# Performance work log

Measured on AMD Instinct MI355X. Metric: run time of the kernel, lower is better.

## Reference

```python
import jax, jax.numpy as jnp
import numpy as np

N = 50000
E = 800000
IN_C = 128
HID = 64
HEADS = 4
NUM_CLASSES = 10
NUM_GRAPHS = 64
EPS = 1e-5
NEG_SLOPE = 0.2


def setup_inputs() -> dict:
    key = jax.random.key(0)
    ks = jax.random.split(key, 32)
    inp = {}
    inp["x"] = jax.random.normal(ks[0], (N, IN_C), dtype=jnp.float32)
    inp["edge_index"] = jax.random.randint(ks[1], (2, E), 0, N, dtype=jnp.int32)
    inp["batch"] = jnp.sort(jax.random.randint(ks[2], (N,), 0, NUM_GRAPHS, dtype=jnp.int32))
    s = 0.05
    # GATConv1: in=128 -> heads=4, hid=64, concat -> 256
    inp["W1"] = jax.random.normal(ks[3], (IN_C, HEADS * HID), dtype=jnp.float32) * s
    inp["a_src1"] = jax.random.normal(ks[4], (HEADS, HID), dtype=jnp.float32) * s
    inp["a_dst1"] = jax.random.normal(ks[5], (HEADS, HID), dtype=jnp.float32) * s
    inp["b1"] = jnp.zeros((HEADS * HID,), dtype=jnp.float32)
    inp["g1"] = jnp.ones((HEADS * HID,), dtype=jnp.float32)
    inp["be1"] = jnp.zeros((HEADS * HID,), dtype=jnp.float32)
    # GATConv2: in=256 -> heads=4, hid=64, concat -> 256
    inp["W2"] = jax.random.normal(ks[6], (HEADS * HID, HEADS * HID), dtype=jnp.float32) * s
    inp["a_src2"] = jax.random.normal(ks[7], (HEADS, HID), dtype=jnp.float32) * s
    inp["a_dst2"] = jax.random.normal(ks[8], (HEADS, HID), dtype=jnp.float32) * s
    inp["b2"] = jnp.zeros((HEADS * HID,), dtype=jnp.float32)
    inp["g2"] = jnp.ones((HEADS * HID,), dtype=jnp.float32)
    inp["be2"] = jnp.zeros((HEADS * HID,), dtype=jnp.float32)
    # GATConv3: in=256 -> heads=1, hid=64, mean (concat=False) -> 64
    inp["W3"] = jax.random.normal(ks[9], (HEADS * HID, 1 * HID), dtype=jnp.float32) * s
    inp["a_src3"] = jax.random.normal(ks[10], (1, HID), dtype=jnp.float32) * s
    inp["a_dst3"] = jax.random.normal(ks[11], (1, HID), dtype=jnp.float32) * s
    inp["b3"] = jnp.zeros((HID,), dtype=jnp.float32)
    inp["g3"] = jnp.ones((HID,), dtype=jnp.float32)
    inp["be3"] = jnp.zeros((HID,), dtype=jnp.float32)
    # final classifier
    inp["fcW"] = jax.random.normal(ks[12], (HID, NUM_CLASSES), dtype=jnp.float32) * s
    inp["fcb"] = jnp.zeros((NUM_CLASSES,), dtype=jnp.float32)
    return inp


def gat_conv(x, src, dst, W, a_src, a_dst, b, heads, out_c, concat):
    # Linear transform, split heads: [N, H, C]
    h = (x @ W).reshape(-1, heads, out_c)
    # Per-node attention logits (dot with per-head attention vectors): [N, H]
    as_ = jnp.einsum("nhc,hc->nh", h, a_src)
    ad_ = jnp.einsum("nhc,hc->nh", h, a_dst)
    # Per-edge unnormalized attention (src contributes a_src, dst a_dst)
    e = jax.nn.leaky_relu(as_[src] + ad_[dst], NEG_SLOPE)  # [E, H]
    # Segment softmax over destination node (stable)
    e_max = jax.ops.segment_max(e, dst, num_segments=N)  # [N, H]
    ex = jnp.exp(e - e_max[dst])
    denom = jax.ops.segment_sum(ex, dst, num_segments=N)  # [N, H]
    alpha = ex / denom[dst]  # [E, H]
    # Weighted scatter-aggregate of source features
    msg = h[src] * alpha[:, :, None]  # [E, H, C]
    out = jax.ops.segment_sum(msg, dst, num_segments=N)  # [N, H, C]
    out = out.reshape(-1, heads * out_c) if concat else out.mean(axis=1)
    return out + b


def batch_norm(x, gamma, beta):
    mean = x.mean(axis=0)
    var = x.var(axis=0)
    return (x - mean) * jax.lax.rsqrt(var + EPS) * gamma + beta


def reference(x, edge_index, batch, W1, a_src1, a_dst1, b1, g1, be1,
              W2, a_src2, a_dst2, b2, g2, be2,
              W3, a_src3, a_dst3, b3, g3, be3, fcW, fcb):
    src, dst = edge_index[0], edge_index[1]
    h = jax.nn.relu(gat_conv(x, src, dst, W1, a_src1, a_dst1, b1, HEADS, HID, True))
    h = batch_norm(h, g1, be1)  # dropout = identity (eval)
    h = jax.nn.relu(gat_conv(h, src, dst, W2, a_src2, a_dst2, b2, HEADS, HID, True))
    h = batch_norm(h, g2, be2)
    h = jax.nn.relu(gat_conv(h, src, dst, W3, a_src3, a_dst3, b3, 1, HID, False))
    h = batch_norm(h, g3, be3)
    # global mean pool over graphs
    sums = jax.ops.segment_sum(h, batch, num_segments=NUM_GRAPHS)  # [G, HID]
    counts = jax.ops.segment_sum(jnp.ones((h.shape[0],), h.dtype), batch, num_segments=NUM_GRAPHS)
    pooled = sums / jnp.maximum(counts, 1.0)[:, None]
    return pooled @ fcW + fcb
```

## Files before the change

### kernel.cpp

```cpp
#include <hip/hip_runtime.h>
#include <hip/hip_bf16.h>

#define N_NODES 50000
#define NUM_E   800000
#define EPS_BN  1e-5f
#define NUM_GRAPHS 64

typedef __attribute__((ext_vector_type(8))) short bf16x8;
typedef __attribute__((ext_vector_type(4))) float f32x4;
typedef unsigned short ushort_t;
typedef unsigned int uint_t;

static __device__ __forceinline__ unsigned short f2bf(float f) {
    unsigned int u = __float_as_uint(f);
    u += 0x7fffu + ((u >> 16) & 1u);
    return (unsigned short)(u >> 16);
}
static __device__ __forceinline__ uint_t pkbf(float lo, float hi) {
    __hip_bfloat162 t = __float22bfloat162_rn(make_float2(lo, hi));
    return *(uint_t*)&t;
}
static __device__ __forceinline__ float bflo(uint_t u) { return __uint_as_float(u << 16); }
static __device__ __forceinline__ float bfhi(uint_t u) { return __uint_as_float(u & 0xffff0000u); }

__global__ void hist_kernel(const int* __restrict__ ei, int* __restrict__ deg) {
    int e = blockIdx.x * blockDim.x + threadIdx.x;
    if (e >= NUM_E) return;
    atomicAdd(&deg[ei[NUM_E + e]], 1);
}

__global__ void scan_local_kernel(const int* __restrict__ deg, int* __restrict__ rowptr,
                                  int* __restrict__ bsum) {
    __shared__ int ws[4];
    int b = blockIdx.x, t = threadIdx.x;
    int i = b * 256 + t;
    int lane = t & 63, wv = t >> 6;
    int v = (i < N_NODES) ? deg[i] : 0;
    int incl = v;
#pragma unroll
    for (int off = 1; off < 64; off <<= 1) {
        int u = __shfl_up(incl, off, 64);
        if (lane >= off) incl += u;
    }
    if (lane == 63) ws[wv] = incl;
    __syncthreads();
    if (t == 0) {
        int s = 0;
#pragma unroll
        for (int k = 0; k < 4; ++k) { int x = ws[k]; ws[k] = s; s += x; }
        bsum[b] = s;
    }
    __syncthreads();
    if (i < N_NODES) rowptr[i + 1] = ws[wv] + incl;
}

__global__ void scan_sums_kernel(int* __restrict__ bsum, int nb) {
    __shared__ int ws[4];
    int t = threadIdx.x;
    int lane = t & 63, wv = t >> 6;
    int v = (t < nb) ? bsum[t] : 0;
    int incl = v;
#pragma unroll
    for (int off = 1; off < 64; off <<= 1) {
        int u = __shfl_up(incl, off, 64);
        if (lane >= off) incl += u;
    }
    if (lane == 63) ws[wv] = incl;
    __syncthreads();
    if (t == 0) {
        int s = 0;
#pragma unroll
        for (int k = 0; k < 4; ++k) { int x = ws[k]; ws[k] = s; s += x; }
    }
    __syncthreads();
    if (t < nb) bsum[t] = ws[wv] + incl - v;
}

__global__ void scan_add_kernel(int* __restrict__ rowptr, const int* __restrict__ bsum) {
    int b = blockIdx.x, t = threadIdx.x;
    int i = b * 256 + t;
    if (i < N_NODES) rowptr[i + 1] += bsum[b];
    if (b == 0 && t == 0) rowptr[0] = 0;
}

__global__ void scatter_kernel(const int* __restrict__ ei, const int* __restrict__ rowptr,
                               int* __restrict__ fill, int* __restrict__ srcs) {
    int e = blockIdx.x * blockDim.x + threadIdx.x;
    if (e >= NUM_E) return;
    int dst = ei[NUM_E + e];
    int pos = rowptr[dst] + atomicAdd(&fill[dst], 1);
    srcs[pos] = ei[e];
}

__global__ void batch_offsets_kernel(const int* __restrict__ batch, int* __restrict__ goff) {
    int g = threadIdx.x;
    if (g > NUM_GRAPHS) return;
    int lo = 0, hi = N_NODES;
    while (lo < hi) {
        int mid = (lo + hi) >> 1;
        if (batch[mid] < g) lo = mid + 1; else hi = mid;
    }
    goff[g] = lo;
}

__global__ void prep_all_kernel(const float* __restrict__ W1, const float* __restrict__ W2,
                                const float* __restrict__ W3, const float* __restrict__ x,
                                ushort_t* __restrict__ w1t, ushort_t* __restrict__ w2t,
                                ushort_t* __restrict__ w3t, ushort_t* __restrict__ xbf) {
    const int S1 = 128 * 256, S2 = 256 * 256, S3 = 256 * 64;
    const int SW = S1 + S2 + S3;
    const int SX = N_NODES * 128 / 4;
    int i = blockIdx.x * blockDim.x + threadIdx.x;
    if (i < SX) {
        float4 v = ((const float4*)x)[i];
        ((uint2*)xbf)[i] = make_uint2(pkbf(v.x, v.y), pkbf(v.z, v.w));
    } else if (i < SX + SW) {
        int j = i - SX;
        if (j < S1) {
            int k = j / 256, n = j % 256;
            w1t[n * 128 + k] = f2bf(W1[j]);
        } else if (j < S1 + S2) {
            int jj = j - S1; int k = jj / 256, n = jj % 256;
            w2t[n * 256 + k] = f2bf(W2[jj]);
        } else {
            int jj = j - S1 - S2; int k = jj / 64, n = jj % 64;
            w3t[n * 256 + k] = f2bf(W3[jj]);
        }
    }
}

__global__ __launch_bounds__(256) void scale_w_kernel(const float* __restrict__ stats,
                                                      const float* __restrict__ g,
                                                      const float* __restrict__ be,
                                                      const ushort_t* __restrict__ wt,
                                                      ushort_t* __restrict__ wts,
                                                      float* __restrict__ cvec) {
    int n = blockIdx.x, k = threadIdx.x;
    float m = stats[k] * (1.f / N_NODES);
    float var = fmaxf(stats[256 + k] * (1.f / N_NODES) - m * m, 0.f);
    float rs = rsqrtf(var + EPS_BN) * g[k];
    float b = be[k] - m * rs;
    float wv = bflo((uint_t)wt[n * 256 + k]);
    wts[n * 256 + k] = f2bf(rs * wv);
    float p = b * wv;
    __shared__ float ws[4];
    int lane = k & 63, wid = k >> 6;
#pragma unroll
    for (int off = 1; off < 64; off <<= 1) p += __shfl_xor(p, off, 64);
    if (lane == 0) ws[wid] = p;
    __syncthreads();
    if (k == 0) cvec[n] = ws[0] + ws[1] + ws[2] + ws[3];
}

template<int K, int NFULL, int BN>
__global__ __launch_bounds__(256) void gemm_fused_kernel(const ushort_t* __restrict__ A,
                                                         const ushort_t* __restrict__ Bt,
                                                         ushort_t* __restrict__ C,
                                                         const float* __restrict__ cvec,
                                                         const float* __restrict__ a_src,
                                                         const float* __restrict__ a_dst,
                                                         float* __restrict__ as_,
                                                         float* __restrict__ ad_) {
    const int NT = BN / 16;
    const int NG = BN / 64;
    constexpr int LOOP_BYTES = (128 * 40 + BN * 40) * 2;
    constexpr int EPI_BYTES  = 4 * 32 * 64 * 2;
    constexpr int SMEM_BYTES = LOOP_BYTES > EPI_BYTES ? LOOP_BYTES : EPI_BYTES;
    __shared__ __align__(16) unsigned char smem[SMEM_BYTES];
    ushort_t (*As)[40]     = (ushort_t (*)[40])smem;
    ushort_t (*Bs)[40]     = (ushort_t (*)[40])(smem + 128 * 40 * 2);
    ushort_t (*Cs)[32][64] = (ushort_t (*)[32][64])smem;
    __shared__ float cvec_s[BN];
    __shared__ float asrc_s[BN], adst_s[BN];
    int tid = threadIdx.x;
    int lane = tid & 63, w = tid >> 6;
    int row0 = blockIdx.x * 128, col0 = blockIdx.y * BN;
    int m_l = lane & 15, q = lane >> 4;

    if (tid < BN) {
        cvec_s[tid] = cvec[col0 + tid];
        asrc_s[tid] = a_src[col0 + tid];
        adst_s[tid] = a_dst[col0 + tid];
    }
    __syncthreads();

    f32x4 acc[2][NT];
#pragma unroll
    for (int r = 0; r < 2; ++r)
#pragma unroll
        for (int c = 0; c < NT; ++c) acc[r][c] = (f32x4){0.f, 0.f, 0.f, 0.f};

    int ar = tid >> 1, ako = (tid & 1) * 16;

    for (int k0 = 0; k0 < K; k0 += 32) {
        int gr = row0 + ar;
        uint4 u0 = make_uint4(0, 0, 0, 0), u1 = make_uint4(0, 0, 0, 0);
        if (gr < N_NODES) {
            const ushort_t* ap = A + (long)gr * K + k0 + ako;
            u0 = *(const uint4*)ap;
            u1 = *(const uint4*)(ap + 8);
        }
        if constexpr (BN == 128) {
            int br = tid >> 1, bko = (tid & 1) * 16;
            const ushort_t* bp = Bt + (long)(col0 + br) * K + k0 + bko;
            uint4 b0 = *(const uint4*)bp;
            uint4 b1 = *(const uint4*)(bp + 8);
            *(uint4*)&As[ar][ako] = u0;
            *(uint4*)&As[ar][ako + 8] = u1;
            *(uint4*)&Bs[br][bko] = b0;
            *(uint4*)&Bs[br][bko + 8] = b1;
        } else {
            int br = tid >> 2, bko = (tid & 3) * 8;
            uint4 bv = *(const uint4*)(Bt + (long)(col0 + br) * K + k0 + bko);
            *(uint4*)&As[ar][ako] = u0;
            *(uint4*)&As[ar][ako + 8] = u1;
            *(uint4*)&Bs[br][bko] = bv;
        }
        __syncthreads();

        bf16x8 af[2];
#pragma unroll
        for (int r = 0; r < 2; ++r)
            af[r] = *(const bf16x8*)&As[w * 32 + r * 16 + m_l][q * 8];
#pragma unroll
        for (int c = 0; c < NT; ++c) {
            bf16x8 bf = *(const bf16x8*)&Bs[c * 16 + m_l][q * 8];
#pragma unroll
            for (int r = 0; r < 2; ++r)
                acc[r][c] = __builtin_amdgcn_mfma_f32_16x16x32_bf16(af[r], bf, acc[r][c], 0, 0, 0);
        }
        __syncthreads();
    }

    const int H = NFULL / 64;
#pragma unroll
    for (int gblk = 0; gblk < NG; ++gblk) {
        int hidx = blockIdx.y * NG + gblk;
        int colg = col0 + gblk * 64;
#pragma unroll
        for (int r = 0; r < 2; ++r)
#pragma unroll
            for (int cc = 0; cc < 4; ++cc)
#pragma unroll
                for (int i = 0; i < 4; ++i)
                    Cs[w][r * 16 + q * 4 + i][cc * 16 + m_l] =
                        f2bf(acc[r][gblk * 4 + cc][i] + cvec_s[gblk * 64 + cc * 16 + m_l]);
#pragma unroll
        for (int j = 0; j < 4; ++j) {
            int flat = j * 64 + lane;
            int lr = flat >> 3, chg = flat & 7;
            int gr = row0 + w * 32 + lr;
            uint4 u = *(uint4*)&Cs[w][lr][chg * 8];
            float f0 = bflo(u.x), f1 = bfhi(u.x), f2 = bflo(u.y), f3 = bfhi(u.y);
            float f4 = bflo(u.z), f5 = bfhi(u.z), f6 = bflo(u.w), f7 = bfhi(u.w);
            int cb = gblk * 64 + chg * 8;
            float s1 = f0 * asrc_s[cb] + f1 * asrc_s[cb + 1] + f2 * asrc_s[cb + 2] + f3 * asrc_s[cb + 3]
                     + f4 * asrc_s[cb + 4] + f5 * asrc_s[cb + 5] + f6 * asrc_s[cb + 6] + f7 * asrc_s[cb + 7];
            float s2 = f0 * adst_s[cb] + f1 * adst_s[cb + 1] + f2 * adst_s[cb + 2] + f3 * adst_s[cb + 3]
                     + f4 * adst_s[cb + 4] + f5 * adst_s[cb + 5] + f6 * adst_s[cb + 6] + f7 * adst_s[cb + 7];
#pragma unroll
            for (int o = 1; o < 8; o <<= 1) {
                s1 += __shfl_xor(s1, o, 64);
                s2 += __shfl_xor(s2, o, 64);
            }
            if (gr < N_NODES) {
                *(uint4*)(C + (long)gr * NFULL + colg + chg * 8) = u;
                if ((lane & 7) == 0) {
                    as_[gr * H + hidx] = s1;
                    ad_[gr * H + hidx] = s2;
                }
            }
        }
    }
}

__global__ __launch_bounds__(256) void agg4_kernel(const ushort_t* __restrict__ h,
                                                   const float* __restrict__ as_,
                                                   const float* __restrict__ ad_,
                                                   const int* __restrict__ rowptr,
                                                   const int* __restrict__ srcs,
                                                   const float* __restrict__ bias,
                                                   ushort_t* __restrict__ out) {
    __shared__ float4 alf[4][4][17];
    __shared__ int    sed[4][4][17];
    int tid = threadIdx.x;
    int lane = tid & 63, w = tid >> 6;
    int q = lane >> 4, cl = lane & 15;
    int n = blockIdx.x * 16 + w * 4 + q;

    int start = rowptr[n];
    int deg = rowptr[n + 1] - start;

    float4 adv = *(const float4*)(ad_ + n * 4);
    float ad4[4] = {adv.x, adv.y, adv.z, adv.w};

    float mx[4] = {-1e30f, -1e30f, -1e30f, -1e30f};
    float dn[4] = {0.f, 0.f, 0.f, 0.f};
    {
        float vst[4] = {-1e30f, -1e30f, -1e30f, -1e30f};
        int s0 = 0;
        if (deg > 0) s0 = srcs[start + min(cl, deg - 1)];
        sed[w][q][cl] = s0;
        if (cl < deg) {
            float4 av = *(const float4*)(as_ + s0 * 4);
            float vv[4] = {av.x + ad4[0], av.y + ad4[1], av.z + ad4[2], av.w + ad4[3]};
#pragma unroll
            for (int hh = 0; hh < 4; ++hh) {
                float v = vv[hh] > 0.f ? vv[hh] : 0.2f * vv[hh];
                vst[hh] = v; mx[hh] = v; dn[hh] = 1.f;
            }
        }
        alf[w][q][cl] = make_float4(vst[0], vst[1], vst[2], vst[3]);
        for (int j = cl + 16; j < deg; j += 16) {
            int s = srcs[start + j];
            float4 av = *(const float4*)(as_ + s * 4);
            float vv[4] = {av.x + ad4[0], av.y + ad4[1], av.z + ad4[2], av.w + ad4[3]};
#pragma unroll
            for (int hh = 0; hh < 4; ++hh) {
                float v = vv[hh] > 0.f ? vv[hh] : 0.2f * vv[hh];
                float mn = fmaxf(mx[hh], v);
                dn[hh] = dn[hh] * __expf(mx[hh] - mn) + __expf(v - mn);
                mx[hh] = mn;
            }
        }
    }
    float mloc[4] = {mx[0], mx[1], mx[2], mx[3]};
#pragma unroll
    for (int off = 1; off < 16; off <<= 1)
#pragma unroll
        for (int hh = 0; hh < 4; ++hh) mx[hh] = fmaxf(mx[hh], __shfl_xor(mx[hh], off, 64));
#pragma unroll
    for (int hh = 0; hh < 4; ++hh) dn[hh] *= __expf(mloc[hh] - mx[hh]);
#pragma unroll
    for (int off = 1; off < 16; off <<= 1)
#pragma unroll
        for (int hh = 0; hh < 4; ++hh) dn[hh] += __shfl_xor(dn[hh], off, 64);
    float inv[4];
#pragma unroll
    for (int hh = 0; hh < 4; ++hh) inv[hh] = dn[hh] > 0.f ? 1.f / dn[hh] : 0.f;
    {
        float4 vv = alf[w][q][cl];
        alf[w][q][cl] = make_float4(__expf(vv.x - mx[0]) * inv[0], __expf(vv.y - mx[1]) * inv[1],
                                    __expf(vv.z - mx[2]) * inv[2], __expf(vv.w - mx[3]) * inv[3]);
    }

    int hd = cl >> 2, cbase = cl * 16;
    float acc[16];
#pragma unroll
    for (int k = 0; k < 16; ++k) acc[k] = 0.f;

    for (int chunk = 0; chunk < deg || chunk == 0; chunk += 16) {
        if (chunk > 0) {
            int j = chunk + cl;
            int s = srcs[start + min(j, deg - 1)];
            sed[w][q][cl] = s;
            float a4[4] = {0.f, 0.f, 0.f, 0.f};
            if (j < deg) {
                float4 av = *(const float4*)(as_ + s * 4);
                float vv[4] = {av.x + ad4[0], av.y + ad4[1], av.z + ad4[2], av.w + ad4[3]};
#pragma unroll
                for (int hh = 0; hh < 4; ++hh) {
                    float v = vv[hh] > 0.f ? vv[hh] : 0.2f * vv[hh];
                    a4[hh] = __expf(v - mx[hh]) * inv[hh];
                }
            }
            alf[w][q][cl] = make_float4(a4[0], a4[1], a4[2], a4[3]);
        }
        int cnt = min(16, deg - chunk);
        if (cnt < 0) cnt = 0;
        int e = 0;
        for (; e + 4 <= cnt; e += 4) {
            float av[4]; int sv[4];
#pragma unroll
            for (int t = 0; t < 4; ++t) {
                av[t] = ((const float*)&alf[w][q][e + t])[hd];
                sv[t] = sed[w][q][e + t];
            }
            uint4 ua[4];
#pragma unroll
            for (int t = 0; t < 4; ++t)
                ua[t] = *(const uint4*)(h + (long)sv[t] * 256 + cbase);
#pragma unroll
            for (int t = 0; t < 4; ++t) {
                float al = av[t];
                acc[0] += al * bflo(ua[t].x); acc[1] += al * bfhi(ua[t].x);
                acc[2] += al * bflo(ua[t].y); acc[3] += al * bfhi(ua[t].y);
                acc[4] += al * bflo(ua[t].z); acc[5] += al * bfhi(ua[t].z);
                acc[6] += al * bflo(ua[t].w); acc[7] += al * bfhi(ua[t].w);
            }
#pragma unroll
            for (int t = 0; t < 4; ++t)
                ua[t] = *(const uint4*)(h + (long)sv[t] * 256 + cbase + 8);
#pragma unroll
            for (int t = 0; t < 4; ++t) {
                float al = av[t];
                acc[8]  += al * bflo(ua[t].x); acc[9]  += al * bfhi(ua[t].x);
                acc[10] += al * bflo(ua[t].y); acc[11] += al * bfhi(ua[t].y);
                acc[12] += al * bflo(ua[t].z); acc[13] += al * bfhi(ua[t].z);
                acc[14] += al * bflo(ua[t].w); acc[15] += al * bfhi(ua[t].w);
            }
        }
        for (; e < cnt; ++e) {
            float al = ((const float*)&alf[w][q][e])[hd];
            const ushort_t* hr = h + (long)sed[w][q][e] * 256 + cbase;
            uint4 u0 = *(const uint4*)hr;
            uint4 u1 = *(const uint4*)(hr + 8);
            acc[0]  += al * bflo(u0.x); acc[1]  += al * bfhi(u0.x);
            acc[2]  += al * bflo(u0.y); acc[3]  += al * bfhi(u0.y);
            acc[4]  += al * bflo(u0.z); acc[5]  += al * bfhi(u0.z);
            acc[6]  += al * bflo(u0.w); acc[7]  += al * bfhi(u0.w);
            acc[8]  += al * bflo(u1.x); acc[9]  += al * bfhi(u1.x);
            acc[10] += al * bflo(u1.y); acc[11] += al * bfhi(u1.y);
            acc[12] += al * bflo(u1.z); acc[13] += al * bfhi(u1.z);
            acc[14] += al * bflo(u1.w); acc[15] += al * bfhi(u1.w);
        }
        if (deg <= 16) break;
    }

    uint_t ow[8];
#pragma unroll
    for (int t = 0; t < 8; ++t) {
        float lo = fmaxf(acc[t * 2] + bias[cbase + t * 2], 0.f);
        float hi = fmaxf(acc[t * 2 + 1] + bias[cbase + t * 2 + 1], 0.f);
        ow[t] = pkbf(lo, hi);
    }
    ushort_t* op = out + (long)n * 256 + cbase;
    *(uint4*)op = make_uint4(ow[0], ow[1], ow[2], ow[3]);
    *(uint4*)(op + 8) = make_uint4(ow[4], ow[5], ow[6], ow[7]);
}

__global__ __launch_bounds__(256) void agg1_kernel(const ushort_t* __restrict__ h,
                                                   const float* __restrict__ as_,
                                                   const float* __restrict__ ad_,
                                                   const int* __restrict__ rowptr,
                                                   const int* __restrict__ srcs,
                                                   const float* __restrict__ bias,
                                                   ushort_t* __restrict__ out,
                                                   float* __restrict__ stats) {
    __shared__ float alf1[4][8][9];
    __shared__ int   sed1[4][8][9];
    __shared__ float ssum[64], ssq[64];
    int tid = threadIdx.x;
    int lane = tid & 63, w = tid >> 6;
    int o = lane >> 3, cl = lane & 7;
    int n = blockIdx.x * 32 + w * 8 + o;
    bool valid = n < N_NODES;
    int nc = valid ? n : N_NODES - 1;
    if (tid < 64) { ssum[tid] = 0.f; ssq[tid] = 0.f; }
    __syncthreads();

    int start = rowptr[nc];
    int deg = valid ? rowptr[nc + 1] - start : 0;
    float adn = ad_[nc];

    float mx = -1e30f, dn = 0.f;
    {
        float vst = -1e30f;
        int s0 = 0;
        if (deg > 0) s0 = srcs[start + min(cl, deg - 1)];
        sed1[w][o][cl] = s0;
        if (cl < deg) {
            float v = as_[s0] + adn;
            v = v > 0.f ? v : 0.2f * v;
            vst = v; mx = v; dn = 1.f;
        }
        alf1[w][o][cl] = vst;
        for (int j = cl + 8; j < deg; j += 8) {
            int s = srcs[start + j];
            float v = as_[s] + adn;
            v = v > 0.f ? v : 0.2f * v;
            float mn = fmaxf(mx, v);
            dn = dn * __expf(mx - mn) + __expf(v - mn);
            mx = mn;
        }
    }
    float mloc = mx;
#pragma unroll
    for (int off = 1; off < 8; off <<= 1) mx = fmaxf(mx, __shfl_xor(mx, off, 64));
    dn *= __expf(mloc - mx);
#pragma unroll
    for (int off = 1; off < 8; off <<= 1) dn += __shfl_xor(dn, off, 64);
    float inv = dn > 0.f ? 1.f / dn : 0.f;

    alf1[w][o][cl] = __expf(alf1[w][o][cl] - mx) * inv;

    int c0 = cl * 8;
    float acc[8] = {0.f, 0.f, 0.f, 0.f, 0.f, 0.f, 0.f, 0.f};

    for (int chunk = 0; chunk < deg || chunk == 0; chunk += 8) {
        if (chunk > 0) {
            int j = chunk + cl;
            int s = srcs[start + min(j, deg - 1)];
            sed1[w][o][cl] = s;
            float al = 0.f;
            if (j < deg) {
                float v = as_[s] + adn;
                v = v > 0.f ? v : 0.2f * v;
                al = __expf(v - mx) * inv;
            }
            alf1[w][o][cl] = al;
        }
        int cnt = min(8, deg - chunk);
        if (cnt < 0) cnt = 0;
        int e = 0;
        for (; e + 4 <= cnt; e += 4) {
            float av[4]; int sv[4];
#pragma unroll
            for (int t = 0; t < 4; ++t) {
                av[t] = alf1[w][o][e + t];
                sv[t] = sed1[w][o][e + t];
            }
            uint4 ua[4];
#pragma unroll
            for (int t = 0; t < 4; ++t)
                ua[t] = *(const uint4*)(h + (long)sv[t] * 64 + c0);
#pragma unroll
            for (int t = 0; t < 4; ++t) {
                float al = av[t];
                acc[0] += al * bflo(ua[t].x); acc[1] += al * bfhi(ua[t].x);
                acc[2] += al * bflo(ua[t].y); acc[3] += al * bfhi(ua[t].y);
                acc[4] += al * bflo(ua[t].z); acc[5] += al * bfhi(ua[t].z);
                acc[6] += al * bflo(ua[t].w); acc[7] += al * bfhi(ua[t].w);
            }
        }
        for (; e < cnt; ++e) {
            float al = alf1[w][o][e];
            uint4 u = *(const uint4*)(h + (long)sed1[w][o][e] * 64 + c0);
            acc[0] += al * bflo(u.x); acc[1] += al * bfhi(u.x);
            acc[2] += al * bflo(u.y); acc[3] += al * bfhi(u.y);
            acc[4] += al * bflo(u.z); acc[5] += al * bfhi(u.z);
            acc[6] += al * bflo(u.w); acc[7] += al * bfhi(u.w);
        }
        if (deg <= 8) break;
    }

    float v[8];
#pragma unroll
    for (int t = 0; t < 8; ++t) v[t] = fmaxf(acc[t] + bias[c0 + t], 0.f);
    if (valid) {
        uint_t ow[4];
#pragma unroll
        for (int t = 0; t < 4; ++t) ow[t] = pkbf(v[2 * t], v[2 * t + 1]);
        *(uint4*)(out + (long)n * 64 + c0) = make_uint4(ow[0], ow[1], ow[2], ow[3]);
    }
    float s1[8], s2[8];
#pragma unroll
    for (int t = 0; t < 8; ++t) {
        s1[t] = valid ? v[t] : 0.f;
        s2[t] = valid ? v[t] * v[t] : 0.f;
    }
#pragma unroll
    for (int off = 8; off < 64; off <<= 1)
#pragma unroll
        for (int t = 0; t < 8; ++t) {
            s1[t] += __shfl_xor(s1[t], off, 64);
            s2[t] += __shfl_xor(s2[t], off, 64);
        }
    if (lane < 8) {
#pragma unroll
        for (int t = 0; t < 8; ++t) {
            atomicAdd(&ssum[c0 + t], s1[t]);
            atomicAdd(&ssq[c0 + t], s2[t]);
        }
    }
    __syncthreads();
    if (tid < 64) {
        atomicAdd(&stats[tid], ssum[tid]);
        atomicAdd(&stats[256 + tid], ssq[tid]);
    }
}

template<int C>
__global__ __launch_bounds__(256) void bn_stats_bf16(const ushort_t* __restrict__ x,
                                                     float* __restrict__ stats) {
    const int GROUPS = C / 8;
    const int RS = 256 / GROUPS;
    int tid = threadIdx.x;
    int cg_ = tid % GROUPS;
    int rs = tid / GROUPS;
    float s[8], s2[8];
#pragma unroll
    for (int k = 0; k < 8; ++k) { s[k] = 0.f; s2[k] = 0.f; }
    for (int n = blockIdx.x * RS + rs; n < N_NODES; n += gridDim.x * RS) {
        uint4 u = *(const uint4*)(x + (long)n * C + cg_ * 8);
        float f[8] = {bflo(u.x), bfhi(u.x), bflo(u.y), bfhi(u.y),
                      bflo(u.z), bfhi(u.z), bflo(u.w), bfhi(u.w)};
#pragma unroll
        for (int k = 0; k < 8; ++k) { s[k] += f[k]; s2[k] += f[k] * f[k]; }
    }
    __shared__ float red[256][16];
#pragma unroll
    for (int k = 0; k < 8; ++k) { red[tid][k] = s[k]; red[tid][8 + k] = s2[k]; }
    __syncthreads();
    if (tid < C) {
        int g = tid >> 3, k = tid & 7;
        float a = 0.f, b = 0.f;
        for (int r = 0; r < RS; ++r) {
            a += red[g + r * GROUPS][k];
            b += red[g + r * GROUPS][8 + k];
        }
        atomicAdd(&stats[tid], a);
        atomicAdd(&stats[256 + tid], b);
    }
}

__global__ __launch_bounds__(256) void pool_fc_kernel(const ushort_t* __restrict__ h,
                                                      const int* __restrict__ goff,
                                                      const float* __restrict__ stats,
                                                      const float* __restrict__ g3,
                                                      const float* __restrict__ be3,
                                                      const float* __restrict__ fcW,
                                                      const float* __restrict__ fcb,
                                                      float* __restrict__ out) {
    int g = blockIdx.x;
    int c = threadIdx.x & 63;
    int ty = threadIdx.x >> 6;
    int s = goff[g], e = goff[g + 1];
    float sum = 0.f;
    for (int n = s + ty; n < e; n += 4) sum += bflo((uint_t)h[(long)n * 64 + c]);
    __shared__ float red[4][64];
    __shared__ float pv[64];
    red[ty][c] = sum;
    __syncthreads();
    if (ty == 0) {
        float tot = red[0][c] + red[1][c] + red[2][c] + red[3][c];
        float v = tot / fmaxf((float)(e - s), 1.f);
        float m = stats[c] * (1.f / N_NODES);
        float var = fmaxf(stats[256 + c] * (1.f / N_NODES) - m * m, 0.f);
        pv[c] = (v - m) * rsqrtf(var + EPS_BN) * g3[c] + be3[c];
    }
    __syncthreads();
    if (threadIdx.x < 10) {
        int j = threadIdx.x;
        float acc = fcb[j];
#pragma unroll
        for (int k = 0; k < 64; ++k) acc += pv[k] * fcW[k * 10 + j];
        out[g * 10 + j] = acc;
    }
}

extern "C" void kernel_launch(void* const* d_in, const int* in_sizes, int n_in,
                              void* d_out, int out_size, void* d_ws, size_t ws_size,
                              hipStream_t stream) {
    const float* x      = (const float*)d_in[0];
    const int*   ei     = (const int*)d_in[1];
    const int*   batch  = (const int*)d_in[2];
    const float* W1     = (const float*)d_in[3];
    const float* a_src1 = (const float*)d_in[4];
    const float* a_dst1 = (const float*)d_in[5];
    const float* b1     = (const float*)d_in[6];
    const float* g1     = (const float*)d_in[7];
    const float* be1    = (const float*)d_in[8];
    const float* W2     = (const float*)d_in[9];
    const float* a_src2 = (const float*)d_in[10];
    const float* a_dst2 = (const float*)d_in[11];
    const float* b2     = (const float*)d_in[12];
    const float* g2     = (const float*)d_in[13];
    const float* be2    = (const float*)d_in[14];
    const float* W3     = (const float*)d_in[15];
    const float* a_src3 = (const float*)d_in[16];
    const float* a_dst3 = (const float*)d_in[17];
    const float* b3     = (const float*)d_in[18];
    const float* g3     = (const float*)d_in[19];
    const float* be3    = (const float*)d_in[20];
    const float* fcW    = (const float*)d_in[21];
    const float* fcb    = (const float*)d_in[22];
    float* out = (float*)d_out;

    const size_t N = N_NODES, E = NUM_E;
    ushort_t* hbf    = (ushort_t*)d_ws;
    ushort_t* hagg   = hbf + N * 256;
    ushort_t* xbf    = hagg + N * 256;
    ushort_t* w1t    = xbf + N * 128;
    ushort_t* w2t    = w1t + 256 * 128;
    ushort_t* w3t    = w2t + 256 * 256;
    ushort_t* w2ts   = w3t + 64 * 256;
    ushort_t* w3ts   = w2ts + 256 * 256;
    float*    as_    = (float*)(w3ts + 64 * 256 + 128);
    float*    ad_    = as_ + N * 4;
    int*      deg    = (int*)(ad_ + N * 4);
    int*      fill   = deg + N;
    float*    statsA = (float*)(fill + N);
    float*    statsB = statsA + 512;
    float*    statsC = statsB + 512;
    float*    cvec0  = statsC + 512;
    int*      rowptr = (int*)(cvec0 + 256);
    int*      srcs   = rowptr + (N + 1);
    int*      bsum   = srcs + E;
    int*      goff   = bsum + 256;
    float*    cvec2  = (float*)(goff + 72);
    float*    cvec3  = cvec2 + 256;

    const int NB = (N_NODES + 255) / 256;

    hipMemsetAsync(deg, 0, sizeof(int) * (2 * N + 3 * 512 + 256), stream);
    hist_kernel<<<(NUM_E + 255) / 256, 256, 0, stream>>>(ei, deg);
    scan_local_kernel<<<NB, 256, 0, stream>>>(deg, rowptr, bsum);
    scan_sums_kernel<<<1, 256, 0, stream>>>(bsum, NB);
    scan_add_kernel<<<NB, 256, 0, stream>>>(rowptr, bsum);
    scatter_kernel<<<(NUM_E + 255) / 256, 256, 0, stream>>>(ei, rowptr, fill, srcs);
    batch_offsets_kernel<<<1, 128, 0, stream>>>(batch, goff);
    prep_all_kernel<<<(N_NODES * 128 / 4 + 128 * 256 + 256 * 256 + 256 * 64 + 255) / 256, 256, 0, stream>>>(
        W1, W2, W3, x, w1t, w2t, w3t, xbf);

    const int GB = (N_NODES + 127) / 128;
    const int AB = N_NODES / 16;

    gemm_fused_kernel<128, 256, 128><<<dim3(GB, 2), 256, 0, stream>>>(
        xbf, w1t, hbf, cvec0, a_src1, a_dst1, as_, ad_);
    agg4_kernel<<<AB, 256, 0, stream>>>(hbf, as_, ad_, rowptr, srcs, b1, hagg);
    bn_stats_bf16<256><<<128, 256, 0, stream>>>(hagg, statsA);

    scale_w_kernel<<<256, 256, 0, stream>>>(statsA, g1, be1, w2t, w2ts, cvec2);
    gemm_fused_kernel<256, 256, 128><<<dim3(GB, 2), 256, 0, stream>>>(
        hagg, w2ts, hbf, cvec2, a_src2, a_dst2, as_, ad_);
    agg4_kernel<<<AB, 256, 0, stream>>>(hbf, as_, ad_, rowptr, srcs, b2, hagg);
    bn_stats_bf16<256><<<128, 256, 0, stream>>>(hagg, statsB);

    scale_w_kernel<<<64, 256, 0, stream>>>(statsB, g2, be2, w3t, w3ts, cvec3);
    gemm_fused_kernel<256, 64, 64><<<dim3(GB, 1), 256, 0, stream>>>(
        hagg, w3ts, hbf, cvec3, a_src3, a_dst3, as_, ad_);
    agg1_kernel<<<(N_NODES + 31) / 32, 256, 0, stream>>>(hbf, as_, ad_, rowptr, srcs, b3, hagg, statsC);

    pool_fc_kernel<<<NUM_GRAPHS, 256, 0, stream>>>(hagg, goff, statsC, g3, be3, fcW, fcb, out);
}
```

Measured before the change: 523.5 us.

## Fuse BN stats into aggregation and merge preprocessing kernels to cut launches

Computes batch-norm sum and sum-of-squares inside agg4_kernel using shuffles, shared atomics and global atomics, which removes the separate bn_stats passes over the aggregated output. The histogram is merged with the weight and input conversion kernel. The three-kernel scan becomes a two-kernel scan, where each block sums the preceding block totals itself. Graph offsets are now found by binary search inside pool_fc, so the batch_offsets kernel goes away. The trade-off is more global atomic traffic on stats (512 atomics per block across 3125 blocks) and redundant prefix sums in the scan.

```diff
diff --git a/kernel.cpp b/kernel.cpp
--- a/kernel.cpp
+++ b/kernel.cpp
@@ -23,94 +23,22 @@
 static __device__ __forceinline__ float bflo(uint_t u) { return __uint_as_float(u << 16); }
 static __device__ __forceinline__ float bfhi(uint_t u) { return __uint_as_float(u & 0xffff0000u); }
 
-__global__ void hist_kernel(const int* __restrict__ ei, int* __restrict__ deg) {
-    int e = blockIdx.x * blockDim.x + threadIdx.x;
-    if (e >= NUM_E) return;
-    atomicAdd(&deg[ei[NUM_E + e]], 1);
-}
-
-__global__ void scan_local_kernel(const int* __restrict__ deg, int* __restrict__ rowptr,
-                                  int* __restrict__ bsum) {
-    __shared__ int ws[4];
-    int b = blockIdx.x, t = threadIdx.x;
-    int i = b * 256 + t;
-    int lane = t & 63, wv = t >> 6;
-    int v = (i < N_NODES) ? deg[i] : 0;
-    int incl = v;
-#pragma unroll
-    for (int off = 1; off < 64; off <<= 1) {
-        int u = __shfl_up(incl, off, 64);
-        if (lane >= off) incl += u;
-    }
-    if (lane == 63) ws[wv] = incl;
-    __syncthreads();
-    if (t == 0) {
-        int s = 0;
-#pragma unroll
-        for (int k = 0; k < 4; ++k) { int x = ws[k]; ws[k] = s; s += x; }
-        bsum[b] = s;
-    }
-    __syncthreads();
-    if (i < N_NODES) rowptr[i + 1] = ws[wv] + incl;
-}
-
-__global__ void scan_sums_kernel(int* __restrict__ bsum, int nb) {
-    __shared__ int ws[4];
-    int t = threadIdx.x;
-    int lane = t & 63, wv = t >> 6;
-    int v = (t < nb) ? bsum[t] : 0;
-    int incl = v;
-#pragma unroll
-    for (int off = 1; off < 64; off <<= 1) {
-        int u = __shfl_up(incl, off, 64);
-        if (lane >= off) incl += u;
-    }
-    if (lane == 63) ws[wv] = incl;
-    __syncthreads();
-    if (t == 0) {
-        int s = 0;
-#pragma unroll
-        for (int k = 0; k < 4; ++k) { int x = ws[k]; ws[k] = s; s += x; }
-    }
-    __syncthreads();
-    if (t < nb) bsum[t] = ws[wv] + incl - v;
-}
-
-__global__ void scan_add_kernel(int* __restrict__ rowptr, const int* __restrict__ bsum) {
-    int b = blockIdx.x, t = threadIdx.x;
-    int i = b * 256 + t;
-    if (i < N_NODES) rowptr[i + 1] += bsum[b];
-    if (b == 0 && t == 0) rowptr[0] = 0;
-}
-
-__global__ void scatter_kernel(const int* __restrict__ ei, const int* __restrict__ rowptr,
-                               int* __restrict__ fill, int* __restrict__ srcs) {
-    int e = blockIdx.x * blockDim.x + threadIdx.x;
-    if (e >= NUM_E) return;
-    int dst = ei[NUM_E + e];
-    int pos = rowptr[dst] + atomicAdd(&fill[dst], 1);
-    srcs[pos] = ei[e];
-}
-
-__global__ void batch_offsets_kernel(const int* __restrict__ batch, int* __restrict__ goff) {
-    int g = threadIdx.x;
-    if (g > NUM_GRAPHS) return;
-    int lo = 0, hi = N_NODES;
-    while (lo < hi) {
-        int mid = (lo + hi) >> 1;
-        if (batch[mid] < g) lo = mid + 1; else hi = mid;
-    }
-    goff[g] = lo;
-}
-
-__global__ void prep_all_kernel(const float* __restrict__ W1, const float* __restrict__ W2,
-                                const float* __restrict__ W3, const float* __restrict__ x,
-                                ushort_t* __restrict__ w1t, ushort_t* __restrict__ w2t,
-                                ushort_t* __restrict__ w3t, ushort_t* __restrict__ xbf) {
+__global__ void hist_prep_kernel(const int* __restrict__ ei, int* __restrict__ deg,
+                                 const float* __restrict__ W1, const float* __restrict__ W2,
+                                 const float* __restrict__ W3, const float* __restrict__ x,
+                                 ushort_t* __restrict__ w1t, ushort_t* __restrict__ w2t,
+                                 ushort_t* __restrict__ w3t, ushort_t* __restrict__ xbf) {
+    const int HB = (NUM_E + 255) / 256;
     const int S1 = 128 * 256, S2 = 256 * 256, S3 = 256 * 64;
     const int SW = S1 + S2 + S3;
     const int SX = N_NODES * 128 / 4;
-    int i = blockIdx.x * blockDim.x + threadIdx.x;
+    int b = blockIdx.x;
+    if (b < HB) {
+        int e = b * 256 + threadIdx.x;
+        if (e < NUM_E) atomicAdd(&deg[ei[NUM_E + e]], 1);
+        return;
+    }
+    int i = (b - HB) * 256 + threadIdx.x;
     if (i < SX) {
         float4 v = ((const float4*)x)[i];
         ((uint2*)xbf)[i] = make_uint2(pkbf(v.x, v.y), pkbf(v.z, v.w));
@@ -127,6 +55,56 @@
             w3t[n * 256 + k] = f2bf(W3[jj]);
         }
     }
+}
+
+__global__ void scan_local_kernel(const int* __restrict__ deg, int* __restrict__ rowptr,
+                                  int* __restrict__ bsum) {
+    __shared__ int ws[4];
+    int b = blockIdx.x, t = threadIdx.x;
+    int i = b * 256 + t;
+    int lane = t & 63, wv = t >> 6;
+    int v = (i < N_NODES) ? deg[i] : 0;
+    int incl = v;
+#pragma unroll
+    for (int off = 1; off < 64; off <<= 1) {
+        int u = __shfl_up(incl, off, 64);
+        if (lane >= off) incl += u;
+    }
+    if (lane == 63) ws[wv] = incl;
+    __syncthreads();
+    if (t == 0) {
+        int s = 0;
+#pragma unroll
+        for (int k = 0; k < 4; ++k) { int x = ws[k]; ws[k] = s; s += x; }
+        bsum[b] = s;
+    }
+    __syncthreads();
+    if (i < N_NODES) rowptr[i + 1] = ws[wv] + incl;
+}
+
+__global__ __launch_bounds__(256) void scan_fixup_kernel(int* __restrict__ rowptr,
+                                                         const int* __restrict__ bsum) {
+    __shared__ int ws[4];
+    int b = blockIdx.x, t = threadIdx.x;
+    int lane = t & 63, wv = t >> 6;
+    int v = (t < b) ? bsum[t] : 0;
+#pragma unroll
+    for (int off = 1; off < 64; off <<= 1) v += __shfl_xor(v, off, 64);
+    if (lane == 0) ws[wv] = v;
+    __syncthreads();
+    int pre = ws[0] + ws[1] + ws[2] + ws[3];
+    int i = b * 256 + t;
+    if (i < N_NODES) rowptr[i + 1] += pre;
+    if (b == 0 && t == 0) rowptr[0] = 0;
+}
+
+__global__ void scatter_kernel(const int* __restrict__ ei, const int* __restrict__ rowptr,
+                               int* __restrict__ fill, int* __restrict__ srcs) {
+    int e = blockIdx.x * blockDim.x + threadIdx.x;
+    if (e >= NUM_E) return;
+    int dst = ei[NUM_E + e];
+    int pos = rowptr[dst] + atomicAdd(&fill[dst], 1);
+    srcs[pos] = ei[e];
 }
 
 __global__ __launch_bounds__(256) void scale_w_kernel(const float* __restrict__ stats,
@@ -280,13 +258,17 @@
                                                    const int* __restrict__ rowptr,
                                                    const int* __restrict__ srcs,
                                                    const float* __restrict__ bias,
-                                                   ushort_t* __restrict__ out) {
+                                                   ushort_t* __restrict__ out,
+                                                   float* __restrict__ stats) {
     __shared__ float4 alf[4][4][17];
     __shared__ int    sed[4][4][17];
+    __shared__ float  ssum[256], ssq[256];
     int tid = threadIdx.x;
     int lane = tid & 63, w = tid >> 6;
     int q = lane >> 4, cl = lane & 15;
     int n = blockIdx.x * 16 + w * 4 + q;
+    ssum[tid] = 0.f; ssq[tid] = 0.f;
+    __syncthreads();
 
     int start = rowptr[n];
     int deg = rowptr[n + 1] - start;
@@ -417,16 +399,28 @@
         if (deg <= 16) break;
     }
 
+#pragma unroll
+    for (int t = 0; t < 16; ++t) acc[t] = fmaxf(acc[t] + bias[cbase + t], 0.f);
     uint_t ow[8];
 #pragma unroll
-    for (int t = 0; t < 8; ++t) {
-        float lo = fmaxf(acc[t * 2] + bias[cbase + t * 2], 0.f);
-        float hi = fmaxf(acc[t * 2 + 1] + bias[cbase + t * 2 + 1], 0.f);
-        ow[t] = pkbf(lo, hi);
-    }
+    for (int t = 0; t < 8; ++t) ow[t] = pkbf(acc[2 * t], acc[2 * t + 1]);
     ushort_t* op = out + (long)n * 256 + cbase;
     *(uint4*)op = make_uint4(ow[0], ow[1], ow[2], ow[3]);
     *(uint4*)(op + 8) = make_uint4(ow[4], ow[5], ow[6], ow[7]);
+
+#pragma unroll
+    for (int t = 0; t < 16; ++t) {
+        float a = acc[t], sq = a * a;
+        a  += __shfl_xor(a, 16, 64);  a  += __shfl_xor(a, 32, 64);
+        sq += __shfl_xor(sq, 16, 64); sq += __shfl_xor(sq, 32, 64);
+        if (lane < 16) {
+            atomicAdd(&ssum[cbase + t], a);
+            atomicAdd(&ssq[cbase + t], sq);
+        }
+    }
+    __syncthreads();
+    atomicAdd(&stats[tid], ssum[tid]);
+    atomicAdd(&stats[256 + tid], ssq[tid]);
 }
 
 __global__ __launch_bounds__(256) void agg1_kernel(const ushort_t* __restrict__ h,
@@ -570,42 +564,8 @@
     }
 }
 
-template<int C>
-__global__ __launch_bounds__(256) void bn_stats_bf16(const ushort_t* __restrict__ x,
-                                                     float* __restrict__ stats) {
-    const int GROUPS = C / 8;
-    const int RS = 256 / GROUPS;
-    int tid = threadIdx.x;
-    int cg_ = tid % GROUPS;
-    int rs = tid / GROUPS;
-    float s[8], s2[8];
-#pragma unroll
-    for (int k = 0; k < 8; ++k) { s[k] = 0.f; s2[k] = 0.f; }
-    for (int n = blockIdx.x * RS + rs; n < N_NODES; n += gridDim.x * RS) {
-        uint4 u = *(const uint4*)(x + (long)n * C + cg_ * 8);
-        float f[8] = {bflo(u.x), bfhi(u.x), bflo(u.y), bfhi(u.y),
-                      bflo(u.z), bfhi(u.z), bflo(u.w), bfhi(u.w)};
-#pragma unroll
-        for (int k = 0; k < 8; ++k) { s[k] += f[k]; s2[k] += f[k] * f[k]; }
-    }
-    __shared__ float red[256][16];
-#pragma unroll
-    for (int k = 0; k < 8; ++k) { red[tid][k] = s[k]; red[tid][8 + k] = s2[k]; }
-    __syncthreads();
-    if (tid < C) {
-        int g = tid >> 3, k = tid & 7;
-        float a = 0.f, b = 0.f;
-        for (int r = 0; r < RS; ++r) {
-            a += red[g + r * GROUPS][k];
-            b += red[g + r * GROUPS][8 + k];
-        }
-        atomicAdd(&stats[tid], a);
-        atomicAdd(&stats[256 + tid], b);
-    }
-}
-
 __global__ __launch_bounds__(256) void pool_fc_kernel(const ushort_t* __restrict__ h,
-                                                      const int* __restrict__ goff,
+                                                      const int* __restrict__ batch,
                                                       const float* __restrict__ stats,
                                                       const float* __restrict__ g3,
                                                       const float* __restrict__ be3,
@@ -613,9 +573,20 @@
                                                       const float* __restrict__ fcb,
                                                       float* __restrict__ out) {
     int g = blockIdx.x;
+    __shared__ int se[2];
+    if (threadIdx.x < 2) {
+        int gg = g + threadIdx.x;
+        int lo = 0, hi = N_NODES;
+        while (lo < hi) {
+            int mid = (lo + hi) >> 1;
+            if (batch[mid] < gg) lo = mid + 1; else hi = mid;
+        }
+        se[threadIdx.x] = lo;
+    }
+    __syncthreads();
+    int s = se[0], e = se[1];
     int c = threadIdx.x & 63;
     int ty = threadIdx.x >> 6;
-    int s = goff[g], e = goff[g + 1];
     float sum = 0.f;
     for (int n = s + ty; n < e; n += 4) sum += bflo((uint_t)h[(long)n * 64 + c]);
     __shared__ float red[4][64];
@@ -687,40 +658,37 @@
     int*      rowptr = (int*)(cvec0 + 256);
     int*      srcs   = rowptr + (N + 1);
     int*      bsum   = srcs + E;
-    int*      goff   = bsum + 256;
-    float*    cvec2  = (float*)(goff + 72);
+    float*    cvec2  = (float*)(bsum + 256);
     float*    cvec3  = cvec2 + 256;
 
     const int NB = (N_NODES + 255) / 256;
+    const int HB = (NUM_E + 255) / 256;
+    const int SX = N_NODES * 128 / 4;
+    const int SW = 128 * 256 + 256 * 256 + 256 * 64;
+    const int PB = (SX + SW + 255) / 256;
 
     hipMemsetAsync(deg, 0, sizeof(int) * (2 * N + 3 * 512 + 256), stream);
-    hist_kernel<<<(NUM_E + 255) / 256, 256, 0, stream>>>(ei, deg);
+    hist_prep_kernel<<<HB + PB, 256, 0, stream>>>(ei, deg, W1, W2, W3, x, w1t, w2t, w3t, xbf);
     scan_local_kernel<<<NB, 256, 0, stream>>>(deg, rowptr, bsum);
-    scan_sums_kernel<<<1, 256, 0, stream>>>(bsum, NB);
-    scan_add_kernel<<<NB, 256, 0, stream>>>(rowptr, bsum);
-    scatter_kernel<<<(NUM_E + 255) / 256, 256, 0, stream>>>(ei, rowptr, fill, srcs);
-    batch_offsets_kernel<<<1, 128, 0, stream>>>(batch, goff);
-    prep_all_kernel<<<(N_NODES * 128 / 4 + 128 * 256 + 256 * 256 + 256 * 64 + 255) / 256, 256, 0, stream>>>(
-        W1, W2, W3, x, w1t, w2t, w3t, xbf);
+    scan_fixup_kernel<<<NB, 256, 0, stream>>>(rowptr, bsum);
+    scatter_kernel<<<HB, 256, 0, stream>>>(ei, rowptr, fill, srcs);
 
     const int GB = (N_NODES + 127) / 128;
     const int AB = N_NODES / 16;
 
     gemm_fused_kernel<128, 256, 128><<<dim3(GB, 2), 256, 0, stream>>>(
         xbf, w1t, hbf, cvec0, a_src1, a_dst1, as_, ad_);
-    agg4_kernel<<<AB, 256, 0, stream>>>(hbf, as_, ad_, rowptr, srcs, b1, hagg);
-    bn_stats_bf16<256><<<128, 256, 0, stream>>>(hagg, statsA);
+    agg4_kernel<<<AB, 256, 0, stream>>>(hbf, as_, ad_, rowptr, srcs, b1, hagg, statsA);
 
     scale_w_kernel<<<256, 256, 0, stream>>>(statsA, g1, be1, w2t, w2ts, cvec2);
     gemm_fused_kernel<256, 256, 128><<<dim3(GB, 2), 256, 0, stream>>>(
         hagg, w2ts, hbf, cvec2, a_src2, a_dst2, as_, ad_);
-    agg4_kernel<<<AB, 256, 0, stream>>>(hbf, as_, ad_, rowptr, srcs, b2, hagg);
-    bn_stats_bf16<256><<<128, 256, 0, stream>>>(hagg, statsB);
+    agg4_kernel<<<AB, 256, 0, stream>>>(hbf, as_, ad_, rowptr, srcs, b2, hagg, statsB);
 
     scale_w_kernel<<<64, 256, 0, stream>>>(statsB, g2, be2, w3t, w3ts, cvec3);
     gemm_fused_kernel<256, 64, 64><<<dim3(GB, 1), 256, 0, stream>>>(
         hagg, w3ts, hbf, cvec3, a_src3, a_dst3, as_, ad_);
     agg1_kernel<<<(N_NODES + 31) / 32, 256, 0, stream>>>(hbf, as_, ad_, rowptr, srcs, b3, hagg, statsC);
 
-    pool_fc_kernel<<<NUM_GRAPHS, 256, 0, stream>>>(hagg, goff, statsC, g3, be3, fcW, fcb, out);
-}
+    pool_fc_kernel<<<NUM_GRAPHS, 256, 0, stream>>>(hagg, batch, statsC, g3, be3, fcW, fcb, out);
+}
```

New measurement: 627.5 us. 19.9% more time.
